# Performance work log

Measured on AMD Instinct MI355X. Metric: run time of the kernel, lower is better.

The kernel has to match this reference:

```python
import jax, jax.numpy as jnp
import numpy as np

IN_F, OUT_F, RANK, BLK = 4096, 4096, 64, 64
N_BLOCKS = min(IN_F, OUT_F) // BLK  # 64


def setup_inputs() -> dict:
    key = jax.random.key(0)
    ks = jax.random.split(key, 6)
    s = 0.02
    x = jax.random.normal(ks[0], (4, 2048, IN_F), dtype=jnp.float32)
    diag_params = jax.random.normal(ks[1], (N_BLOCKS, IN_F // N_BLOCKS, OUT_F // N_BLOCKS), dtype=jnp.float32) * s
    W_left = jax.random.normal(ks[2], (RANK, IN_F), dtype=jnp.float32) * s   # torch Linear weight [out,in]
    W_right = jax.random.normal(ks[3], (OUT_F, RANK), dtype=jnp.float32) * s
    b_right = jax.random.normal(ks[4], (OUT_F,), dtype=jnp.float32) * s
    bias = jax.random.normal(ks[5], (OUT_F,), dtype=jnp.float32) * s
    return {"x": x, "diag_params": diag_params, "W_left": W_left,
            "W_right": W_right, "b_right": b_right, "bias": bias}


def reference(x, diag_params, W_left, W_right, b_right, bias):
    nb, bi, bo = diag_params.shape
    lead = x.shape[:-1]
    # block-diagonal matmul: x @ block_diag(*diag_params), without materializing the dense matrix
    xb = x.reshape(*lead, nb, bi)                       # [..., nb, bi]
    x1 = jnp.einsum('...nd,ndo->...no', xb, diag_params).reshape(*lead, nb * bo)
    # low-rank path: right(left(x)) with right's bias
    x2 = (x @ W_left.T) @ W_right.T + b_right
    return x1 + x2 + bias
```

## Files before the change

kernel.cpp:

```cpp
#include <hip/hip_runtime.h>
#include <hip/hip_bf16.h>
#include <stdint.h>


#define M_TOT   8192
#define IN_F    4096
#define OUT_F   4096
#define RANK    64
#define NBLK    64

typedef __attribute__((ext_vector_type(8))) short  bf16x8;
typedef __attribute__((ext_vector_type(4))) float  floatx4;

#define WS_BIAS   0
#define WS_WL     16384
#define WS_BP     540672

#define S_TP 68

__device__ __forceinline__ unsigned short f2bf(float f) {
    union { float f; unsigned int u; } v; v.f = f;
    unsigned int u = v.u;
    u += 0x7fffu + ((u >> 16) & 1u);
    return (unsigned short)(u >> 16);
}

__device__ __forceinline__ bf16x8 cvt8(floatx4 a0, floatx4 a1) {
    bf16x8 af;
    af[0] = (short)f2bf(a0[0]); af[1] = (short)f2bf(a0[1]);
    af[2] = (short)f2bf(a0[2]); af[3] = (short)f2bf(a0[3]);
    af[4] = (short)f2bf(a1[0]); af[5] = (short)f2bf(a1[1]);
    af[6] = (short)f2bf(a1[2]); af[7] = (short)f2bf(a1[3]);
    return af;
}

__global__ __launch_bounds__(256) void prep_kernel(
    const float* __restrict__ diag, const float* __restrict__ Wl,
    const float* __restrict__ Wr,   const float* __restrict__ br,
    const float* __restrict__ bias,
    float* __restrict__ bias_comb, unsigned short* __restrict__ wl_pack,
    unsigned short* __restrict__ bp_pack)
{
    int tid = blockIdx.x * blockDim.x + threadIdx.x;
    int nthr = gridDim.x * blockDim.x;

    for (int i = tid; i < OUT_F; i += nthr)
        bias_comb[i] = br[i] + bias[i];

    for (int i = tid; i < 64 * 4096; i += nthr) {
        int n = i >> 12, c = i & 4095;
        wl_pack[(((size_t)(c >> 5) * 4 + (n >> 4)) * 64
                 + ((c >> 3) & 3) * 16 + (n & 15)) * 8 + (c & 7)] = f2bf(Wl[i]);
    }

    for (int i = tid; i < 64 * 64 * 64; i += nthr) {
        int nb = i >> 12, k = (i >> 6) & 63, n = i & 63;
        bp_pack[((((size_t)nb * 4 + (k >> 5)) * 4 + (n >> 4)) * 64
                 + ((k >> 3) & 3) * 16 + (n & 15)) * 8 + (k & 7)] = f2bf(diag[i]);
    }

    for (int i = tid; i < 64 * 64 * 64; i += nthr) {
        int nb = i >> 12, n = (i >> 6) & 63, r = i & 63;
        bp_pack[((((size_t)nb * 4 + 2 + (r >> 5)) * 4 + (n >> 4)) * 64
                 + ((r >> 3) & 3) * 16 + (n & 15)) * 8 + (r & 7)] = f2bf(Wr[i]);
    }
}

__global__ __launch_bounds__(512, 4) void fused_kernel(
    const float* __restrict__ x, const unsigned short* __restrict__ wl_pack,
    const unsigned short* __restrict__ bp_pack, const float* __restrict__ bias_comb,
    float* __restrict__ out)
{
    __shared__ float t_part[8 * 16 * S_TP];

    int w = threadIdx.x >> 6;
    int lane = threadIdx.x & 63;
    int q = lane >> 4, l = lane & 15;
    int mt = blockIdx.x;
    int m0 = mt * 16;
    int kc_g0 = w * 16;

    const float* xrow = x + (size_t)(m0 + l) * IN_F + q * 8;

    bf16x8 xfrag[16];
    floatx4 tacc[4] = {};

    #pragma unroll
    for (int kc = 0; kc < 16; ++kc) {
        int kc_g = kc_g0 + kc;
        const float* ap = xrow + kc_g * 32;
        floatx4 a0 = __builtin_nontemporal_load((const floatx4*)(ap));
        floatx4 a1 = __builtin_nontemporal_load((const floatx4*)(ap + 4));
        bf16x8 af = cvt8(a0, a1);
        xfrag[kc] = af;
        #pragma unroll
        for (int nt = 0; nt < 4; ++nt) {
            bf16x8 bf = *(const bf16x8*)(wl_pack +
                (((size_t)kc_g * 4 + nt) * 64 + lane) * 8);
            tacc[nt] = __builtin_amdgcn_mfma_f32_16x16x32_bf16(af, bf, tacc[nt], 0, 0, 0);
        }
    }

    #pragma unroll
    for (int nt = 0; nt < 4; ++nt)
        #pragma unroll
        for (int r = 0; r < 4; ++r)
            t_part[w * 16 * S_TP + (q * 4 + r) * S_TP + nt * 16 + l] = tacc[nt][r];

    __syncthreads();

    bf16x8 tfrag[2];
    #pragma unroll
    for (int kc2 = 0; kc2 < 2; ++kc2) {
        floatx4 s0 = {0.f, 0.f, 0.f, 0.f}, s1 = {0.f, 0.f, 0.f, 0.f};
        #pragma unroll
        for (int p = 0; p < 8; ++p) {
            const float* tp = &t_part[p * 16 * S_TP + l * S_TP + kc2 * 32 + q * 8];
            floatx4 v0 = *(const floatx4*)(tp);
            floatx4 v1 = *(const floatx4*)(tp + 4);
            s0 += v0;
            s1 += v1;
        }
        tfrag[kc2] = cvt8(s0, s1);
    }

    __syncthreads();

    float* sw = &t_part[w * 16 * S_TP];
    int hi = lane >> 4, lo = lane & 15;

    #pragma unroll
    for (int i = 0; i < 8; ++i) {
        int nb = w * 8 + i;

        floatx4 acc[4];
        #pragma unroll
        for (int nt = 0; nt < 4; ++nt) {
            float bv = bias_comb[nb * 64 + nt * 16 + l];
            acc[nt][0] = bv; acc[nt][1] = bv; acc[nt][2] = bv; acc[nt][3] = bv;
        }

        #pragma unroll
        for (int kc = 0; kc < 4; ++kc) {
            bf16x8 af = (kc < 2) ? xfrag[2 * i + kc] : tfrag[kc - 2];
            #pragma unroll
            for (int nt = 0; nt < 4; ++nt) {
                bf16x8 bf = *(const bf16x8*)(bp_pack +
                    ((((size_t)nb * 4 + kc) * 4 + nt) * 64 + lane) * 8);
                acc[nt] = __builtin_amdgcn_mfma_f32_16x16x32_bf16(af, bf, acc[nt], 0, 0, 0);
            }
        }

        #pragma unroll
        for (int nt = 0; nt < 4; ++nt)
            #pragma unroll
            for (int r = 0; r < 4; ++r)
                sw[(q * 4 + r) * S_TP + nt * 16 + l] = acc[nt][r];

        #pragma unroll
        for (int c = 0; c < 4; ++c) {
            int row = c * 4 + hi;
            floatx4 v = *(const floatx4*)&sw[row * S_TP + lo * 4];
            __builtin_nontemporal_store(v,
                (floatx4*)(out + (size_t)(m0 + row) * OUT_F + nb * 64 + lo * 4));
        }
    }
}

extern "C" void kernel_launch(void* const* d_in, const int* in_sizes, int n_in,
                              void* d_out, int out_size, void* d_ws, size_t ws_size,
                              hipStream_t stream) {
    const float* x    = (const float*)d_in[0];
    const float* diag = (const float*)d_in[1];
    const float* Wl   = (const float*)d_in[2];
    const float* Wr   = (const float*)d_in[3];
    const float* br   = (const float*)d_in[4];
    const float* bias = (const float*)d_in[5];
    float* out = (float*)d_out;

    char* ws = (char*)d_ws;
    float*          bias_comb = (float*)(ws + WS_BIAS);
    unsigned short* wl_pack   = (unsigned short*)(ws + WS_WL);
    unsigned short* bp_pack   = (unsigned short*)(ws + WS_BP);

    hipLaunchKernelGGL(prep_kernel, dim3(512), dim3(256), 0, stream,
                       diag, Wl, Wr, br, bias, bias_comb, wl_pack, bp_pack);
    hipLaunchKernelGGL(fused_kernel, dim3(512), dim3(512), 0, stream,
                       x, wl_pack, bp_pack, bias_comb, out);
}
```

Baseline: 268.5 us.

## Process 32 rows per block to reuse weight fragments across two M tiles

Each workgroup now handles 32 rows instead of 16, loading each W_left and packed block-diagonal/W_right fragment once and using it for two MFMA row tiles. The grid halves to 256 blocks and shared memory doubles, with occupancy hint lowered to 2. This cuts weight traffic from global/L2 per output row. In exchange register pressure doubles (xfrag 32 vectors), and with only 256 blocks on a 256-CU part each CU gets a single block, so there is less latency hiding.

```diff
diff --git a/kernel.cpp b/kernel.cpp
--- a/kernel.cpp
+++ b/kernel.cpp
@@ -66,99 +66,116 @@
     }
 }
 
-__global__ __launch_bounds__(512, 4) void fused_kernel(
+__global__ __launch_bounds__(512, 2) void fused_kernel(
     const float* __restrict__ x, const unsigned short* __restrict__ wl_pack,
     const unsigned short* __restrict__ bp_pack, const float* __restrict__ bias_comb,
     float* __restrict__ out)
 {
-    __shared__ float t_part[8 * 16 * S_TP];
+    __shared__ float t_part[8 * 32 * S_TP];
 
     int w = threadIdx.x >> 6;
     int lane = threadIdx.x & 63;
     int q = lane >> 4, l = lane & 15;
     int mt = blockIdx.x;
-    int m0 = mt * 16;
+    int m0 = mt * 32;
     int kc_g0 = w * 16;
 
-    const float* xrow = x + (size_t)(m0 + l) * IN_F + q * 8;
-
-    bf16x8 xfrag[16];
-    floatx4 tacc[4] = {};
+    bf16x8 xfrag[2][16];
+    floatx4 tacc[2][4] = {};
 
     #pragma unroll
     for (int kc = 0; kc < 16; ++kc) {
         int kc_g = kc_g0 + kc;
-        const float* ap = xrow + kc_g * 32;
-        floatx4 a0 = __builtin_nontemporal_load((const floatx4*)(ap));
-        floatx4 a1 = __builtin_nontemporal_load((const floatx4*)(ap + 4));
-        bf16x8 af = cvt8(a0, a1);
-        xfrag[kc] = af;
-        #pragma unroll
-        for (int nt = 0; nt < 4; ++nt) {
-            bf16x8 bf = *(const bf16x8*)(wl_pack +
+        bf16x8 bfw[4];
+        #pragma unroll
+        for (int nt = 0; nt < 4; ++nt)
+            bfw[nt] = *(const bf16x8*)(wl_pack +
                 (((size_t)kc_g * 4 + nt) * 64 + lane) * 8);
-            tacc[nt] = __builtin_amdgcn_mfma_f32_16x16x32_bf16(af, bf, tacc[nt], 0, 0, 0);
-        }
-    }
-
-    #pragma unroll
-    for (int nt = 0; nt < 4; ++nt)
-        #pragma unroll
-        for (int r = 0; r < 4; ++r)
-            t_part[w * 16 * S_TP + (q * 4 + r) * S_TP + nt * 16 + l] = tacc[nt][r];
+
+        #pragma unroll
+        for (int h = 0; h < 2; ++h) {
+            const float* ap = x + (size_t)(m0 + h * 16 + l) * IN_F + q * 8 + kc_g * 32;
+            floatx4 a0 = __builtin_nontemporal_load((const floatx4*)(ap));
+            floatx4 a1 = __builtin_nontemporal_load((const floatx4*)(ap + 4));
+            bf16x8 af = cvt8(a0, a1);
+            xfrag[h][kc] = af;
+            #pragma unroll
+            for (int nt = 0; nt < 4; ++nt)
+                tacc[h][nt] = __builtin_amdgcn_mfma_f32_16x16x32_bf16(af, bfw[nt], tacc[h][nt], 0, 0, 0);
+        }
+    }
+
+    #pragma unroll
+    for (int h = 0; h < 2; ++h)
+        #pragma unroll
+        for (int nt = 0; nt < 4; ++nt)
+            #pragma unroll
+            for (int r = 0; r < 4; ++r)
+                t_part[(w * 32 + h * 16 + q * 4 + r) * S_TP + nt * 16 + l] = tacc[h][nt][r];
 
     __syncthreads();
 
-    bf16x8 tfrag[2];
-    #pragma unroll
-    for (int kc2 = 0; kc2 < 2; ++kc2) {
-        floatx4 s0 = {0.f, 0.f, 0.f, 0.f}, s1 = {0.f, 0.f, 0.f, 0.f};
-        #pragma unroll
-        for (int p = 0; p < 8; ++p) {
-            const float* tp = &t_part[p * 16 * S_TP + l * S_TP + kc2 * 32 + q * 8];
-            floatx4 v0 = *(const floatx4*)(tp);
-            floatx4 v1 = *(const floatx4*)(tp + 4);
-            s0 += v0;
-            s1 += v1;
-        }
-        tfrag[kc2] = cvt8(s0, s1);
-    }
+    bf16x8 tfrag[2][2];
+    #pragma unroll
+    for (int h = 0; h < 2; ++h)
+        #pragma unroll
+        for (int kc2 = 0; kc2 < 2; ++kc2) {
+            floatx4 s0 = {0.f, 0.f, 0.f, 0.f}, s1 = {0.f, 0.f, 0.f, 0.f};
+            #pragma unroll
+            for (int p = 0; p < 8; ++p) {
+                const float* tp = &t_part[(p * 32 + h * 16 + l) * S_TP + kc2 * 32 + q * 8];
+                floatx4 v0 = *(const floatx4*)(tp);
+                floatx4 v1 = *(const floatx4*)(tp + 4);
+                s0 += v0;
+                s1 += v1;
+            }
+            tfrag[h][kc2] = cvt8(s0, s1);
+        }
 
     __syncthreads();
 
-    float* sw = &t_part[w * 16 * S_TP];
+    float* sw = &t_part[w * 32 * S_TP];
     int hi = lane >> 4, lo = lane & 15;
 
     #pragma unroll
     for (int i = 0; i < 8; ++i) {
         int nb = w * 8 + i;
 
-        floatx4 acc[4];
+        floatx4 acc[2][4];
         #pragma unroll
         for (int nt = 0; nt < 4; ++nt) {
             float bv = bias_comb[nb * 64 + nt * 16 + l];
-            acc[nt][0] = bv; acc[nt][1] = bv; acc[nt][2] = bv; acc[nt][3] = bv;
+            #pragma unroll
+            for (int h = 0; h < 2; ++h) {
+                acc[h][nt][0] = bv; acc[h][nt][1] = bv;
+                acc[h][nt][2] = bv; acc[h][nt][3] = bv;
+            }
         }
 
         #pragma unroll
         for (int kc = 0; kc < 4; ++kc) {
-            bf16x8 af = (kc < 2) ? xfrag[2 * i + kc] : tfrag[kc - 2];
             #pragma unroll
             for (int nt = 0; nt < 4; ++nt) {
                 bf16x8 bf = *(const bf16x8*)(bp_pack +
                     ((((size_t)nb * 4 + kc) * 4 + nt) * 64 + lane) * 8);
-                acc[nt] = __builtin_amdgcn_mfma_f32_16x16x32_bf16(af, bf, acc[nt], 0, 0, 0);
+                #pragma unroll
+                for (int h = 0; h < 2; ++h) {
+                    bf16x8 af = (kc < 2) ? xfrag[h][2 * i + kc] : tfrag[h][kc - 2];
+                    acc[h][nt] = __builtin_amdgcn_mfma_f32_16x16x32_bf16(af, bf, acc[h][nt], 0, 0, 0);
+                }
             }
         }
 
         #pragma unroll
-        for (int nt = 0; nt < 4; ++nt)
-            #pragma unroll
-            for (int r = 0; r < 4; ++r)
-                sw[(q * 4 + r) * S_TP + nt * 16 + l] = acc[nt][r];
-
-        #pragma unroll
-        for (int c = 0; c < 4; ++c) {
+        for (int h = 0; h < 2; ++h)
+            #pragma unroll
+            for (int nt = 0; nt < 4; ++nt)
+                #pragma unroll
+                for (int r = 0; r < 4; ++r)
+                    sw[(h * 16 + q * 4 + r) * S_TP + nt * 16 + l] = acc[h][nt][r];
+
+        #pragma unroll
+        for (int c = 0; c < 8; ++c) {
             int row = c * 4 + hi;
             floatx4 v = *(const floatx4*)&sw[row * S_TP + lo * 4];
             __builtin_nontemporal_store(v,
@@ -185,6 +202,6 @@
 
     hipLaunchKernelGGL(prep_kernel, dim3(512), dim3(256), 0, stream,
                        diag, Wl, Wr, br, bias, bias_comb, wl_pack, bp_pack);
-    hipLaunchKernelGGL(fused_kernel, dim3(512), dim3(512), 0, stream,
+    hipLaunchKernelGGL(fused_kernel, dim3(256), dim3(512), 0, stream,
                        x, wl_pack, bp_pack, bias_comb, out);
 }
```

After: 267.1 us. No clear change (-0.5%).

## Process two row tiles per block, overlapping second tile's low-rank GEMM with first's output

Applied to the files above, without the earlier changes.

Each workgroup now handles 32 rows instead of 16, as two 16-row tiles. The x loads and left-projection MFMAs for the second tile are interleaved into the first tile's block-diagonal output loop, hiding load latency behind compute. The grid halves to 256 blocks, launch bounds drop to 2 waves/SIMD, the LDS buffer doubles, and output stores switch from nontemporal to regular. Register pressure doubles (two xfrag sets), and fewer blocks may underfill the 256 CUs.

```diff
diff --git a/kernel.cpp b/kernel.cpp
--- a/kernel.cpp
+++ b/kernel.cpp
@@ -17,6 +17,7 @@
 #define WS_BP     540672
 
 #define S_TP 68
+#define TBUF (8 * 16 * S_TP)
 
 __device__ __forceinline__ unsigned short f2bf(float f) {
     union { float f; unsigned int u; } v; v.f = f;
@@ -66,83 +67,94 @@
     }
 }
 
-__global__ __launch_bounds__(512, 4) void fused_kernel(
+__global__ __launch_bounds__(512, 2) void fused_kernel(
     const float* __restrict__ x, const unsigned short* __restrict__ wl_pack,
     const unsigned short* __restrict__ bp_pack, const float* __restrict__ bias_comb,
     float* __restrict__ out)
 {
-    __shared__ float t_part[8 * 16 * S_TP];
+    __shared__ float t_part[2 * TBUF];
 
     int w = threadIdx.x >> 6;
     int lane = threadIdx.x & 63;
     int q = lane >> 4, l = lane & 15;
-    int mt = blockIdx.x;
-    int m0 = mt * 16;
+    int m0 = blockIdx.x * 32;
     int kc_g0 = w * 16;
 
-    const float* xrow = x + (size_t)(m0 + l) * IN_F + q * 8;
-
-    bf16x8 xfrag[16];
-    floatx4 tacc[4] = {};
-
-    #pragma unroll
-    for (int kc = 0; kc < 16; ++kc) {
-        int kc_g = kc_g0 + kc;
-        const float* ap = xrow + kc_g * 32;
-        floatx4 a0 = __builtin_nontemporal_load((const floatx4*)(ap));
-        floatx4 a1 = __builtin_nontemporal_load((const floatx4*)(ap + 4));
-        bf16x8 af = cvt8(a0, a1);
-        xfrag[kc] = af;
-        #pragma unroll
-        for (int nt = 0; nt < 4; ++nt) {
-            bf16x8 bf = *(const bf16x8*)(wl_pack +
-                (((size_t)kc_g * 4 + nt) * 64 + lane) * 8);
-            tacc[nt] = __builtin_amdgcn_mfma_f32_16x16x32_bf16(af, bf, tacc[nt], 0, 0, 0);
-        }
-    }
-
-    #pragma unroll
-    for (int nt = 0; nt < 4; ++nt)
-        #pragma unroll
-        for (int r = 0; r < 4; ++r)
-            t_part[w * 16 * S_TP + (q * 4 + r) * S_TP + nt * 16 + l] = tacc[nt][r];
+    bf16x8 xfrag[2][16];
+    bf16x8 tfrag[2][2];
+
+    {
+        floatx4 tacc0[4] = {};
+        #pragma unroll
+        for (int kc = 0; kc < 16; ++kc) {
+            int kc_g = kc_g0 + kc;
+            const float* ap = x + (size_t)(m0 + l) * IN_F + q * 8 + kc_g * 32;
+            floatx4 a0 = __builtin_nontemporal_load((const floatx4*)(ap));
+            floatx4 a1 = __builtin_nontemporal_load((const floatx4*)(ap + 4));
+            bf16x8 af = cvt8(a0, a1);
+            xfrag[0][kc] = af;
+            #pragma unroll
+            for (int nt = 0; nt < 4; ++nt) {
+                bf16x8 bf = *(const bf16x8*)(wl_pack +
+                    (((size_t)kc_g * 4 + nt) * 64 + lane) * 8);
+                tacc0[nt] = __builtin_amdgcn_mfma_f32_16x16x32_bf16(af, bf, tacc0[nt], 0, 0, 0);
+            }
+        }
+        #pragma unroll
+        for (int nt = 0; nt < 4; ++nt)
+            #pragma unroll
+            for (int r = 0; r < 4; ++r)
+                t_part[(w * 16 + q * 4 + r) * S_TP + nt * 16 + l] = tacc0[nt][r];
+    }
 
     __syncthreads();
 
-    bf16x8 tfrag[2];
     #pragma unroll
     for (int kc2 = 0; kc2 < 2; ++kc2) {
         floatx4 s0 = {0.f, 0.f, 0.f, 0.f}, s1 = {0.f, 0.f, 0.f, 0.f};
         #pragma unroll
         for (int p = 0; p < 8; ++p) {
-            const float* tp = &t_part[p * 16 * S_TP + l * S_TP + kc2 * 32 + q * 8];
-            floatx4 v0 = *(const floatx4*)(tp);
-            floatx4 v1 = *(const floatx4*)(tp + 4);
-            s0 += v0;
-            s1 += v1;
-        }
-        tfrag[kc2] = cvt8(s0, s1);
+            const float* tp = &t_part[(p * 16 + l) * S_TP + kc2 * 32 + q * 8];
+            s0 += *(const floatx4*)(tp);
+            s1 += *(const floatx4*)(tp + 4);
+        }
+        tfrag[0][kc2] = cvt8(s0, s1);
     }
 
     __syncthreads();
 
     float* sw = &t_part[w * 16 * S_TP];
-    int hi = lane >> 4, lo = lane & 15;
+    floatx4 tacc1[4] = {};
 
     #pragma unroll
     for (int i = 0; i < 8; ++i) {
+        #pragma unroll
+        for (int kk = 0; kk < 2; ++kk) {
+            int kc = 2 * i + kk;
+            int kc_g = kc_g0 + kc;
+            const float* ap = x + (size_t)(m0 + 16 + l) * IN_F + q * 8 + kc_g * 32;
+            floatx4 a0 = __builtin_nontemporal_load((const floatx4*)(ap));
+            floatx4 a1 = __builtin_nontemporal_load((const floatx4*)(ap + 4));
+            bf16x8 af = cvt8(a0, a1);
+            xfrag[1][kc] = af;
+            #pragma unroll
+            for (int nt = 0; nt < 4; ++nt) {
+                bf16x8 bf = *(const bf16x8*)(wl_pack +
+                    (((size_t)kc_g * 4 + nt) * 64 + lane) * 8);
+                tacc1[nt] = __builtin_amdgcn_mfma_f32_16x16x32_bf16(af, bf, tacc1[nt], 0, 0, 0);
+            }
+        }
+
         int nb = w * 8 + i;
-
         floatx4 acc[4];
         #pragma unroll
         for (int nt = 0; nt < 4; ++nt) {
             float bv = bias_comb[nb * 64 + nt * 16 + l];
             acc[nt][0] = bv; acc[nt][1] = bv; acc[nt][2] = bv; acc[nt][3] = bv;
         }
-
         #pragma unroll
         for (int kc = 0; kc < 4; ++kc) {
-            bf16x8 af = (kc < 2) ? xfrag[2 * i + kc] : tfrag[kc - 2];
+            bf16x8 af = (kc < 2) ? xfrag[0][2 * i + kc] : tfrag[0][kc - 2];
             #pragma unroll
             for (int nt = 0; nt < 4; ++nt) {
                 bf16x8 bf = *(const bf16x8*)(bp_pack +
@@ -150,19 +162,68 @@
                 acc[nt] = __builtin_amdgcn_mfma_f32_16x16x32_bf16(af, bf, acc[nt], 0, 0, 0);
             }
         }
-
         #pragma unroll
         for (int nt = 0; nt < 4; ++nt)
             #pragma unroll
             for (int r = 0; r < 4; ++r)
                 sw[(q * 4 + r) * S_TP + nt * 16 + l] = acc[nt][r];
-
         #pragma unroll
         for (int c = 0; c < 4; ++c) {
-            int row = c * 4 + hi;
-            floatx4 v = *(const floatx4*)&sw[row * S_TP + lo * 4];
-            __builtin_nontemporal_store(v,
-                (floatx4*)(out + (size_t)(m0 + row) * OUT_F + nb * 64 + lo * 4));
+            int row = c * 4 + q;
+            floatx4 v = *(const floatx4*)&sw[row * S_TP + l * 4];
+            *(floatx4*)(out + (size_t)(m0 + row) * OUT_F + nb * 64 + l * 4) = v;
+        }
+    }
+
+    #pragma unroll
+    for (int nt = 0; nt < 4; ++nt)
+        #pragma unroll
+        for (int r = 0; r < 4; ++r)
+            t_part[TBUF + (w * 16 + q * 4 + r) * S_TP + nt * 16 + l] = tacc1[nt][r];
+
+    __syncthreads();
+
+    #pragma unroll
+    for (int kc2 = 0; kc2 < 2; ++kc2) {
+        floatx4 s0 = {0.f, 0.f, 0.f, 0.f}, s1 = {0.f, 0.f, 0.f, 0.f};
+        #pragma unroll
+        for (int p = 0; p < 8; ++p) {
+            const float* tp = &t_part[TBUF + (p * 16 + l) * S_TP + kc2 * 32 + q * 8];
+            s0 += *(const floatx4*)(tp);
+            s1 += *(const floatx4*)(tp + 4);
+        }
+        tfrag[1][kc2] = cvt8(s0, s1);
+    }
+
+    #pragma unroll
+    for (int i = 0; i < 8; ++i) {
+        int nb = w * 8 + i;
+        floatx4 acc[4];
+        #pragma unroll
+        for (int nt = 0; nt < 4; ++nt) {
+            float bv = bias_comb[nb * 64 + nt * 16 + l];
+            acc[nt][0] = bv; acc[nt][1] = bv; acc[nt][2] = bv; acc[nt][3] = bv;
+        }
+        #pragma unroll
+        for (int kc = 0; kc < 4; ++kc) {
+            bf16x8 af = (kc < 2) ? xfrag[1][2 * i + kc] : tfrag[1][kc - 2];
+            #pragma unroll
+            for (int nt = 0; nt < 4; ++nt) {
+                bf16x8 bf = *(const bf16x8*)(bp_pack +
+                    ((((size_t)nb * 4 + kc) * 4 + nt) * 64 + lane) * 8);
+                acc[nt] = __builtin_amdgcn_mfma_f32_16x16x32_bf16(af, bf, acc[nt], 0, 0, 0);
+            }
+        }
+        #pragma unroll
+        for (int nt = 0; nt < 4; ++nt)
+            #pragma unroll
+            for (int r = 0; r < 4; ++r)
+                sw[(q * 4 + r) * S_TP + nt * 16 + l] = acc[nt][r];
+        #pragma unroll
+        for (int c = 0; c < 4; ++c) {
+            int row = c * 4 + q;
+            floatx4 v = *(const floatx4*)&sw[row * S_TP + l * 4];
+            *(floatx4*)(out + (size_t)(m0 + 16 + row) * OUT_F + nb * 64 + l * 4) = v;
         }
     }
 }
@@ -185,6 +246,6 @@
 
     hipLaunchKernelGGL(prep_kernel, dim3(512), dim3(256), 0, stream,
                        diag, Wl, Wr, br, bias, bias_comb, wl_pack, bp_pack);
-    hipLaunchKernelGGL(fused_kernel, dim3(512), dim3(512), 0, stream,
+    hipLaunchKernelGGL(fused_kernel, dim3(256), dim3(512), 0, stream,
                        x, wl_pack, bp_pack, bias_comb, out);
 }
```

Measured after the change: 331.2 us. 23.3% more time.
